# Optimization experiments

Hardware: AMD Instinct MI355X
Metric: run time of the kernel (lower is better)

## Reference

```python
import jax, jax.numpy as jnp
import numpy as np

BS, S, DIM, H = 4, 2048, 1024, 16
DH = DIM // H  # 64


def setup_inputs() -> dict:
    key = jax.random.key(0)
    ks = jax.random.split(key, 12)
    def lin(k, fan_in):
        bound = 1.0 / np.sqrt(fan_in)
        kw, kb = jax.random.split(k)
        W = jax.random.uniform(kw, (DIM, DIM), jnp.float32, -bound, bound)
        b = jax.random.uniform(kb, (DIM,), jnp.float32, -bound, bound)
        return W, b
    Wq, bq = lin(ks[0], DIM)
    Wk, bk = lin(ks[1], DIM)
    Wv, bv = lin(ks[2], DIM)
    Wo, bo = lin(ks[3], DIM)
    return {
        "query": jax.random.normal(ks[4], (BS, S, DIM), jnp.float32),
        "key": jax.random.normal(ks[5], (BS, S, DIM), jnp.float32),
        "value": jax.random.normal(ks[6], (BS, S, DIM), jnp.float32),
        "mask": jnp.ones((BS, S), jnp.int32),
        "Wq": Wq, "bq": bq, "Wk": Wk, "bk": bk,
        "Wv": Wv, "bv": bv, "Wo": Wo, "bo": bo,
    }


def reference(query, key, value, mask, Wq, bq, Wk, bk, Wv, bv, Wo, bo):
    bs, q_len, dim = query.shape
    def shape_heads(x):  # (bs, s, dim) -> (bs, H, s, DH)
        return x.reshape(bs, -1, H, DH).transpose(0, 2, 1, 3)
    # Linear projections (torch Linear: x @ W.T + b)
    q = shape_heads(query @ Wq.T + bq)
    k = shape_heads(key @ Wk.T + bk)
    v = shape_heads(value @ Wv.T + bv)
    q = q / jnp.sqrt(jnp.asarray(DH, q.dtype))
    # scores: (bs, H, q_len, k_len)
    scores = jnp.einsum('bhqd,bhkd->bhqk', q, k)
    neg = jnp.asarray(-jnp.inf, scores.dtype)
    pad = (mask == 0)[:, None, None, :]  # (bs,1,1,k_len)
    scores = jnp.where(pad, neg, scores)
    weights = jax.nn.softmax(scores, axis=-1)
    # dropout is identity in eval mode (reference is deterministic)
    context = jnp.einsum('bhqk,bhkd->bhqd', weights, v)
    context = context.transpose(0, 2, 1, 3).reshape(bs, q_len, dim)
    return context @ Wo.T + bo
```

## Files before the change

kernel.cpp:

```cpp
#include <hip/hip_runtime.h>
#include <hip/hip_bf16.h>
#include <math.h>

#define BSZ 4
#define SEQ 2048
#define DIMN 1024
#define NHEAD 16
#define DHEAD 64
#define MROWS (BSZ*SEQ)

typedef __bf16 bf16x8 __attribute__((ext_vector_type(8)));
typedef float  f32x4  __attribute__((ext_vector_type(4)));
typedef float  f32x16 __attribute__((ext_vector_type(16)));
typedef float  fvec4  __attribute__((ext_vector_type(4)));
typedef short  s16x4  __attribute__((ext_vector_type(4)));
typedef short  s16x8  __attribute__((ext_vector_type(8)));

__device__ __forceinline__ short f2bf(float v) {
  __hip_bfloat16 b = __float2bfloat16(v);
  return *reinterpret_cast<short*>(&b);
}
__device__ __forceinline__ float bf2f(short s) {
  __hip_bfloat16 b = *reinterpret_cast<__hip_bfloat16*>(&s);
  return __bfloat162float(b);
}

__device__ __forceinline__ void gld_lds16(const void* g, void* l) {
  __builtin_amdgcn_global_load_lds((const __attribute__((address_space(1))) void*)g,
                                   (__attribute__((address_space(3))) void*)l, 16, 0, 0);
}

#define QSC 0.18033688011112042f

__global__ __launch_bounds__(256) void pack_w4(
    const float* __restrict__ Wq, const float* __restrict__ Wk,
    const float* __restrict__ Wv, const float* __restrict__ Wo,
    short* __restrict__ WQh, short* __restrict__ WKh,
    short* __restrict__ WVh, short* __restrict__ WOh, short* __restrict__ WOl,
    long n)
{
  long i = ((long)blockIdx.x * 256 + threadIdx.x) * 4;
  if (i >= n) return;
  int which = blockIdx.y;
  if (which == 3) {
    fvec4 v = *(const fvec4*)&Wo[i];
    s16x4 h, l;
#pragma unroll
    for (int j = 0; j < 4; ++j) {
      short hb = f2bf(v[j]);
      h[j] = hb;
      l[j] = f2bf(v[j] - bf2f(hb));
    }
    *(s16x4*)&WOh[i] = h;
    *(s16x4*)&WOl[i] = l;
  } else {
    const float* src = which == 0 ? Wq : (which == 1 ? Wk : Wv);
    short* dst = which == 0 ? WQh : (which == 1 ? WKh : WVh);
    float sc = which == 0 ? QSC : 1.f;
    fvec4 v = *(const fvec4*)&src[i];
    s16x4 h;
#pragma unroll
    for (int j = 0; j < 4; ++j) h[j] = f2bf(v[j] * sc);
    *(s16x4*)&dst[i] = h;
  }
}

__global__ __launch_bounds__(256) void pack_hi3(
    const float* __restrict__ q, const float* __restrict__ k,
    const float* __restrict__ v,
    short* __restrict__ xq, short* __restrict__ xk, short* __restrict__ xv,
    long n)
{
  long i = ((long)blockIdx.x * 256 + threadIdx.x) * 4;
  if (i >= n) return;
  const float* src = blockIdx.y == 0 ? q : (blockIdx.y == 1 ? k : v);
  short* dst = blockIdx.y == 0 ? xq : (blockIdx.y == 1 ? xk : xv);
  fvec4 x = *(const fvec4*)&src[i];
  s16x4 h;
#pragma unroll
  for (int j = 0; j < 4; ++j) h[j] = f2bf(x[j]);
  *(s16x4*)&dst[i] = h;
}

__global__ __launch_bounds__(256) void maskbias_k(
    const int* __restrict__ mask, float* __restrict__ mb, int n)
{
  int i = blockIdx.x * 256 + threadIdx.x;
  if (i < n) mb[i] = mask[i] ? 0.f : -1e30f;
}

__global__ __launch_bounds__(64) void mask_flags(
    const int* __restrict__ mask, int* __restrict__ flg)
{
  int c = blockIdx.x;
  int base = (c >> 4) * SEQ + (c & 15) * 128;
  int m0 = mask[base + threadIdx.x];
  int m1 = mask[base + 64 + threadIdx.x];
  unsigned long long bal = __ballot(m0 != 0 && m1 != 0);
  if (threadIdx.x == 0) flg[c] = (bal == ~0ull) ? 1 : 0;
}

__global__ __launch_bounds__(256) void gemm_qkv(
    const short* __restrict__ XBq, const short* __restrict__ XBk,
    const short* __restrict__ XBv,
    const short* __restrict__ WQh, const short* __restrict__ WKh,
    const short* __restrict__ WVh,
    const float* __restrict__ bq, const float* __restrict__ bk,
    const float* __restrict__ bv,
    short* __restrict__ QB, short* __restrict__ KB, short* __restrict__ VTo)
{
  __shared__ __align__(16) short sA[128*32];
  __shared__ __align__(16) short sB[128*32];
  const int z = blockIdx.z;
  const short* A  = z == 0 ? XBq : (z == 1 ? XBk : XBv);
  const short* Bw = z == 0 ? WQh : (z == 1 ? WKh : WVh);
  const float* bias = z == 0 ? bq : (z == 1 ? bk : bv);
  short* Cb = z == 0 ? QB : (z == 1 ? KB : VTo);
  const float bscale = z == 0 ? QSC : 1.f;

  const int flat = blockIdx.y * 8 + blockIdx.x;
  const int nb = (flat & 7) * 64 + (flat >> 3);
  const int m0 = (nb >> 3) * 128, n0 = (nb & 7) * 128;

  const int t = threadIdx.x;
  const int ln = t & 15, quad = (t & 63) >> 4, w = t >> 6;
  const int wm = w >> 1, wn = w & 1;
  const int lrow = t >> 2;
  const int lko = (((t & 3) ^ ((t >> 3) & 3))) * 8;
  const int fsw = ((ln >> 1) & 3);
  f32x4 acc[4][4];
#pragma unroll
  for (int i = 0; i < 4; ++i)
#pragma unroll
    for (int j = 0; j < 4; ++j) acc[i][j] = (f32x4){0.f,0.f,0.f,0.f};

  for (int k0 = 0; k0 < DIMN; k0 += 32) {
    __syncthreads();
#pragma unroll
    for (int u = 0; u < 2; ++u) {
      int row = u*64 + lrow;
      gld_lds16(A  + (size_t)(m0+row)*DIMN + k0 + lko, sA + u*2048 + t*8);
      gld_lds16(Bw + (size_t)(n0+row)*DIMN + k0 + lko, sB + u*2048 + t*8);
    }
    __syncthreads();
    bf16x8 af[4], bfr[4];
#pragma unroll
    for (int mt = 0; mt < 4; ++mt)
      af[mt] = *(bf16x8*)&sA[(wm*64 + mt*16 + ln)*32 + (quad ^ fsw)*8];
#pragma unroll
    for (int nt = 0; nt < 4; ++nt)
      bfr[nt] = *(bf16x8*)&sB[(wn*64 + nt*16 + ln)*32 + (quad ^ fsw)*8];
#pragma unroll
    for (int mt = 0; mt < 4; ++mt)
#pragma unroll
      for (int nt = 0; nt < 4; ++nt)
        acc[mt][nt] = __builtin_amdgcn_mfma_f32_16x16x32_bf16(af[mt], bfr[nt], acc[mt][nt], 0, 0, 0);
  }
#pragma unroll
  for (int nt = 0; nt < 4; ++nt) {
    int col = n0 + wn*64 + nt*16 + ln;
    float bv2 = bias[col] * bscale;
    if (z == 2) {
      int hd = col >> 6, dd = col & 63;
#pragma unroll
      for (int mt = 0; mt < 4; ++mt) {
        int sg = m0 + wm*64 + mt*16 + quad*4;
        int b = sg >> 11, s = sg & 2047;
        s16x4 h;
#pragma unroll
        for (int r = 0; r < 4; ++r) h[r] = f2bf(acc[mt][nt][r] + bv2);
        *(s16x4*)&Cb[((size_t)((b*16 + hd)*64 + dd))*SEQ + s] = h;
      }
    } else {
#pragma unroll
      for (int mt = 0; mt < 4; ++mt)
#pragma unroll
        for (int r = 0; r < 4; ++r) {
          int row = m0 + wm*64 + mt*16 + quad*4 + r;
          Cb[(size_t)row*DIMN + col] = f2bf(acc[mt][nt][r] + bv2);
        }
    }
  }
}

__global__ __launch_bounds__(256) void gemm_sp(
    const short* __restrict__ Ah, const short* __restrict__ Al,
    const short* __restrict__ Bh, const short* __restrict__ Bl,
    const float* __restrict__ bias, float bscale,
    float* __restrict__ C, int M, int N, int K)
{
  __shared__ __align__(16) short sA[2*128*32];
  __shared__ __align__(16) short sB[2*128*32];
  const int t = threadIdx.x;
  const int ln = t & 15, quad = (t & 63) >> 4, w = t >> 6;
  const int wm = w >> 1, wn = w & 1;
  const int flat = blockIdx.y * 8 + blockIdx.x;
  const int nb = (flat & 7) * 64 + (flat >> 3);
  const int m0 = (nb >> 3) * 128, n0 = (nb & 7) * 128;
  const int lrow = t >> 2;
  const int lko = (((t & 3) ^ ((t >> 3) & 3))) * 8;
  const int fsw = ((ln >> 1) & 3);
  f32x4 acc[4][4];
#pragma unroll
  for (int i = 0; i < 4; ++i)
#pragma unroll
    for (int j = 0; j < 4; ++j) acc[i][j] = (f32x4){0.f,0.f,0.f,0.f};

  for (int k0 = 0; k0 < K; k0 += 32) {
    __syncthreads();
#pragma unroll
    for (int u = 0; u < 2; ++u) {
      int row = u*64 + lrow;
      gld_lds16(Ah + (size_t)(m0+row)*K + k0 + lko, sA + u*2048 + t*8);
      gld_lds16(Al + (size_t)(m0+row)*K + k0 + lko, sA + 4096 + u*2048 + t*8);
      gld_lds16(Bh + (size_t)(n0+row)*K + k0 + lko, sB + u*2048 + t*8);
      gld_lds16(Bl + (size_t)(n0+row)*K + k0 + lko, sB + 4096 + u*2048 + t*8);
    }
    __syncthreads();
    bf16x8 ah[4], al[4], bh[4], bl[4];
#pragma unroll
    for (int mt = 0; mt < 4; ++mt) {
      int r = wm*64 + mt*16 + ln;
      ah[mt] = *(bf16x8*)&sA[r*32 + (quad ^ fsw)*8];
      al[mt] = *(bf16x8*)&sA[4096 + r*32 + (quad ^ fsw)*8];
    }
#pragma unroll
    for (int nt = 0; nt < 4; ++nt) {
      int r = wn*64 + nt*16 + ln;
      bh[nt] = *(bf16x8*)&sB[r*32 + (quad ^ fsw)*8];
      bl[nt] = *(bf16x8*)&sB[4096 + r*32 + (quad ^ fsw)*8];
    }
#pragma unroll
    for (int mt = 0; mt < 4; ++mt)
#pragma unroll
      for (int nt = 0; nt < 4; ++nt) {
        acc[mt][nt] = __builtin_amdgcn_mfma_f32_16x16x32_bf16(ah[mt], bh[nt], acc[mt][nt], 0, 0, 0);
        acc[mt][nt] = __builtin_amdgcn_mfma_f32_16x16x32_bf16(ah[mt], bl[nt], acc[mt][nt], 0, 0, 0);
        acc[mt][nt] = __builtin_amdgcn_mfma_f32_16x16x32_bf16(al[mt], bh[nt], acc[mt][nt], 0, 0, 0);
      }
  }
#pragma unroll
  for (int nt = 0; nt < 4; ++nt) {
    float bv = bias[n0 + wn*64 + nt*16 + ln] * bscale;
#pragma unroll
    for (int mt = 0; mt < 4; ++mt)
#pragma unroll
      for (int r = 0; r < 4; ++r)
        C[(size_t)(m0 + wm*64 + mt*16 + quad*4 + r)*N + (n0 + wn*64 + nt*16 + ln)] =
            acc[mt][nt][r] + bv;
  }
}

__global__ __launch_bounds__(256, 3) void attn_32(
    const short* __restrict__ QB, const short* __restrict__ KB,
    const short* __restrict__ VT, const float* __restrict__ mb,
    const int* __restrict__ flg,
    short* __restrict__ CTXh, short* __restrict__ CTXl)
{
  __shared__ __align__(16) short lds[16384];
  short* sK = lds;
  short* sV = lds + 8192;

  const int t = threadIdx.x;
  const int l31 = t & 31, hi = (t >> 5) & 1, w = t >> 6;
  const int gb = blockIdx.x;
  const int chunk = gb >> 3, qt128 = chunk & 15, bh = ((chunk >> 4) << 3) + (gb & 7);
  const int b = bh >> 4, hd = bh & 15;

#pragma unroll
  for (int i = 0; i < 4; ++i) {
    int u = i*256 + t;
    int row = u >> 3, gr = (u & 7) ^ (row & 7);
    gld_lds16(QB + ((size_t)(b*SEQ + qt128*128 + row))*DIMN + hd*64 + gr*8,
              sK + u*8);
  }
  __syncthreads();
  const int q = w*32 + l31;
  bf16x8 qf[4];
#pragma unroll
  for (int ks = 0; ks < 4; ++ks)
    qf[ks] = *(bf16x8*)&sK[q*64 + ((ks*2 + hi) ^ (q & 7))*8];

  f32x16 o_acc[2] = {};
  float m_run = -1e30f, l_run = 0.f;

  for (int kt = 0; kt < SEQ/128; ++kt) {
    __syncthreads();
#pragma unroll
    for (int i = 0; i < 4; ++i) {
      int u = i*256 + t;
      { int row = u >> 3, gr = (u & 7) ^ (row & 7);
        gld_lds16(KB + ((size_t)(b*SEQ + kt*128 + row))*DIMN + hd*64 + gr*8,
                  sK + u*8); }
      { int d = u >> 4, gr = (u & 15) ^ (d & 15);
        gld_lds16(VT + ((size_t)(bh*64 + d))*SEQ + kt*128 + gr*8,
                  sV + u*8); }
    }
    __syncthreads();

    f32x16 sacc[4] = {};
#pragma unroll
    for (int ks = 0; ks < 4; ++ks)
#pragma unroll
      for (int mt = 0; mt < 4; ++mt) {
        int kc = mt*32 + l31;
        bf16x8 kf = *(bf16x8*)&sK[kc*64 + ((ks*2 + hi) ^ (kc & 7))*8];
        sacc[mt] = __builtin_amdgcn_mfma_f32_32x32x16_bf16(kf, qf[ks], sacc[mt], 0, 0, 0);
      }

    if (!flg[b*16 + kt]) {
#pragma unroll
      for (int mt = 0; mt < 4; ++mt)
#pragma unroll
        for (int r = 0; r < 16; ++r)
          sacc[mt][r] += mb[b*SEQ + kt*128 + mt*32 + (r&3) + 8*(r>>2) + 4*hi];
    }

    float tmax = -1e30f;
#pragma unroll
    for (int mt = 0; mt < 4; ++mt)
#pragma unroll
      for (int r = 0; r < 16; ++r) tmax = fmaxf(tmax, sacc[mt][r]);
    tmax = fmaxf(tmax, __shfl_xor(tmax, 32));

    if (!__all(tmax <= m_run + 8.f)) {
      float mnew = fmaxf(m_run, tmax);
      float alpha = exp2f(m_run - mnew);
      l_run *= alpha;
#pragma unroll
      for (int dt = 0; dt < 2; ++dt)
#pragma unroll
        for (int r = 0; r < 16; ++r) o_acc[dt][r] *= alpha;
      m_run = mnew;
    }

    float rs = 0.f;
#pragma unroll
    for (int mt = 0; mt < 4; ++mt)
#pragma unroll
      for (int r = 0; r < 16; ++r) {
        float p = exp2f(sacc[mt][r] - m_run);
        sacc[mt][r] = p;
        rs += p;
      }
    rs += __shfl_xor(rs, 32);
    l_run += rs;

#pragma unroll
    for (int mt = 0; mt < 4; ++mt) {
      unsigned wv[8];
#pragma unroll
      for (int i = 0; i < 8; ++i) {
        float plo = sacc[mt][2*i], phi = sacc[mt][2*i+1];
        asm("v_cvt_pk_bf16_f32 %0, %1, %2" : "=v"(wv[i]) : "v"(plo), "v"(phi));
      }
#pragma unroll
      for (int h = 0; h < 2; ++h) {
        unsigned f0 = wv[h*4+0], f1 = wv[h*4+1], f2 = wv[h*4+2], f3 = wv[h*4+3];
        asm volatile("v_permlane32_swap_b32 %0, %1" : "+v"(f0), "+v"(f2));
        asm volatile("v_permlane32_swap_b32 %0, %1" : "+v"(f1), "+v"(f3));
        union { unsigned u[4]; bf16x8 v; } pu;
        pu.u[0] = f0; pu.u[1] = f1; pu.u[2] = f2; pu.u[3] = f3;
        const int kcs = mt*2 + h;
#pragma unroll
        for (int dt = 0; dt < 2; ++dt) {
          int d = dt*32 + l31;
          bf16x8 vf = *(bf16x8*)&sV[d*128 + ((kcs*2 + hi) ^ (d & 15))*8];
          o_acc[dt] = __builtin_amdgcn_mfma_f32_32x32x16_bf16(vf, pu.v, o_acc[dt], 0, 0, 0);
        }
      }
    }
  }

  float invl = (l_run > 0.f) ? 1.f / l_run : 0.f;
  const size_t rowbase = (size_t)(b*SEQ + qt128*128 + q)*DIMN + hd*64;
#pragma unroll
  for (int dt = 0; dt < 2; ++dt)
#pragma unroll
    for (int rg = 0; rg < 4; ++rg) {
      s16x4 hq, lq;
#pragma unroll
      for (int r2 = 0; r2 < 4; ++r2) {
        float val = o_acc[dt][rg*4 + r2] * invl;
        short hb = f2bf(val);
        hq[r2] = hb;
        lq[r2] = f2bf(val - bf2f(hb));
      }
      size_t idx = rowbase + dt*32 + rg*8 + hi*4;
      *(s16x4*)&CTXh[idx] = hq;
      *(s16x4*)&CTXl[idx] = lq;
    }
}

__global__ __launch_bounds__(256) void gemm_bt(
    const float* __restrict__ X, const float* __restrict__ W,
    const float* __restrict__ bias, float* __restrict__ C,
    int M, int N, int K)
{
  __shared__ __align__(16) float Xs[16][68];
  __shared__ __align__(16) float Ws[16][68];
  const int t  = threadIdx.x;
  const int tx = t & 15, ty = t >> 4;
  const int m0 = blockIdx.y << 6, n0 = blockIdx.x << 6;
  const int ldr = t >> 2;
  const int lk  = (t & 3) << 2;
  float acc[4][4] = {{0.f}};
  const float* Xp = X + (size_t)(m0 + ldr) * K + lk;
  const float* Wp = W + (size_t)(n0 + ldr) * K + lk;
  for (int k0 = 0; k0 < K; k0 += 16) {
    float4 xa = *(const float4*)(Xp + k0);
    float4 wa = *(const float4*)(Wp + k0);
    Xs[lk+0][ldr]=xa.x; Xs[lk+1][ldr]=xa.y; Xs[lk+2][ldr]=xa.z; Xs[lk+3][ldr]=xa.w;
    Ws[lk+0][ldr]=wa.x; Ws[lk+1][ldr]=wa.y; Ws[lk+2][ldr]=wa.z; Ws[lk+3][ldr]=wa.w;
    __syncthreads();
#pragma unroll
    for (int kk = 0; kk < 16; ++kk) {
      float4 a4 = *(const float4*)&Xs[kk][ty<<2];
      float4 b4 = *(const float4*)&Ws[kk][tx<<2];
      float av[4] = {a4.x, a4.y, a4.z, a4.w};
      float bv[4] = {b4.x, b4.y, b4.z, b4.w};
#pragma unroll
      for (int i = 0; i < 4; ++i)
#pragma unroll
        for (int j = 0; j < 4; ++j)
          acc[i][j] = fmaf(av[i], bv[j], acc[i][j]);
    }
    __syncthreads();
  }
  float4 bb4 = *(const float4*)&bias[n0 + (tx<<2)];
  const float bv[4] = {bb4.x, bb4.y, bb4.z, bb4.w};
#pragma unroll
  for (int i = 0; i < 4; ++i) {
    float4 o;
    o.x = acc[i][0]+bv[0]; o.y = acc[i][1]+bv[1];
    o.z = acc[i][2]+bv[2]; o.w = acc[i][3]+bv[3];
    *(float4*)&C[(size_t)(m0 + (ty<<2) + i) * N + n0 + (tx<<2)] = o;
  }
}

__global__ __launch_bounds__(256) void attn_fwd(
    const float* __restrict__ Q, const float* __restrict__ Kbuf,
    const float* __restrict__ Vbuf, const int* __restrict__ mask,
    float* __restrict__ CTX)
{
  __shared__ __align__(16) float Qs[64][68];
  __shared__ __align__(16) float KPs[64][68];
  __shared__ __align__(16) float Vs[64][68];
  const int t  = threadIdx.x;
  const int tx = t & 15, ty = t >> 4;
  const int qt = blockIdx.x;
  const int bh = blockIdx.y;
  const int b  = bh >> 4, h = bh & 15;
  const int ldr = t >> 2;
  const int lcb = (t & 3) << 2;
  const float* Qp = Q + (size_t)(b*SEQ + (qt<<6)) * DIMN + h*DHEAD;
#pragma unroll
  for (int u = 0; u < 4; ++u) {
    int kb = lcb + (u<<4);
    float4 q4 = *(const float4*)(Qp + (size_t)ldr*DIMN + kb);
    Qs[kb+0][ldr]=q4.x; Qs[kb+1][ldr]=q4.y; Qs[kb+2][ldr]=q4.z; Qs[kb+3][ldr]=q4.w;
  }
  float mrow[4], lsum[4], o[4][4];
#pragma unroll
  for (int i = 0; i < 4; ++i) {
    mrow[i] = -1e30f; lsum[i] = 0.f;
#pragma unroll
    for (int j = 0; j < 4; ++j) o[i][j] = 0.f;
  }
  const int qrow0 = ty << 2;
  const int col0  = tx << 2;
  for (int kt = 0; kt < SEQ/64; ++kt) {
    __syncthreads();
    const float* Kp = Kbuf + (size_t)(b*SEQ + (kt<<6)) * DIMN + h*DHEAD;
    const float* Vp = Vbuf + (size_t)(b*SEQ + (kt<<6)) * DIMN + h*DHEAD;
#pragma unroll
    for (int u = 0; u < 4; ++u) {
      int kb = lcb + (u<<4);
      float4 k4 = *(const float4*)(Kp + (size_t)ldr*DIMN + kb);
      KPs[kb+0][ldr]=k4.x; KPs[kb+1][ldr]=k4.y; KPs[kb+2][ldr]=k4.z; KPs[kb+3][ldr]=k4.w;
      float4 v4 = *(const float4*)(Vp + (size_t)ldr*DIMN + kb);
      *(float4*)&Vs[ldr][kb] = v4;
    }
    __syncthreads();
    float s[4][4] = {{0.f}};
#pragma unroll 8
    for (int kk = 0; kk < 64; ++kk) {
      float4 a4 = *(const float4*)&Qs[kk][qrow0];
      float4 b4 = *(const float4*)&KPs[kk][col0];
      float av[4] = {a4.x, a4.y, a4.z, a4.w};
      float bv[4] = {b4.x, b4.y, b4.z, b4.w};
#pragma unroll
      for (int i = 0; i < 4; ++i)
#pragma unroll
        for (int j = 0; j < 4; ++j)
          s[i][j] = fmaf(av[i], bv[j], s[i][j]);
    }
    int mk[4];
#pragma unroll
    for (int j = 0; j < 4; ++j) mk[j] = mask[b*SEQ + (kt<<6) + col0 + j];
    float p[4][4];
#pragma unroll
    for (int i = 0; i < 4; ++i) {
#pragma unroll
      for (int j = 0; j < 4; ++j)
        s[i][j] = mk[j] ? s[i][j]*0.125f : -1e30f;
      float tm = fmaxf(fmaxf(s[i][0], s[i][1]), fmaxf(s[i][2], s[i][3]));
#pragma unroll
      for (int off = 8; off >= 1; off >>= 1)
        tm = fmaxf(tm, __shfl_xor(tm, off, 64));
      float mnew  = fmaxf(mrow[i], tm);
      float aa = __expf(mrow[i] - mnew);
      mrow[i] = mnew;
      float rsum = 0.f;
#pragma unroll
      for (int j = 0; j < 4; ++j) {
        float pv = __expf(s[i][j] - mnew);
        p[i][j] = pv; rsum += pv;
      }
#pragma unroll
      for (int off = 8; off >= 1; off >>= 1)
        rsum += __shfl_xor(rsum, off, 64);
      lsum[i] = lsum[i]*aa + rsum;
#pragma unroll
      for (int j = 0; j < 4; ++j) o[i][j] *= aa;
    }
    __syncthreads();
#pragma unroll
    for (int i = 0; i < 4; ++i)
#pragma unroll
      for (int j = 0; j < 4; ++j)
        KPs[col0 + j][qrow0 + i] = p[i][j];
    __syncthreads();
#pragma unroll 8
    for (int kk = 0; kk < 64; ++kk) {
      float4 a4 = *(const float4*)&KPs[kk][qrow0];
      float4 v4 = *(const float4*)&Vs[kk][col0];
      float av[4] = {a4.x, a4.y, a4.z, a4.w};
      float vv[4] = {v4.x, v4.y, v4.z, v4.w};
#pragma unroll
      for (int i = 0; i < 4; ++i)
#pragma unroll
        for (int j = 0; j < 4; ++j)
          o[i][j] = fmaf(av[i], vv[j], o[i][j]);
    }
  }
  float* Cp = CTX + (size_t)(b*SEQ + (qt<<6)) * DIMN + h*DHEAD;
#pragma unroll
  for (int i = 0; i < 4; ++i) {
    float inv = lsum[i] > 0.f ? 1.0f/lsum[i] : 0.f;
    float4 ov;
    ov.x = o[i][0]*inv; ov.y = o[i][1]*inv;
    ov.z = o[i][2]*inv; ov.w = o[i][3]*inv;
    *(float4*)(Cp + (size_t)(qrow0 + i)*DIMN + col0) = ov;
  }
}

extern "C" void kernel_launch(void* const* d_in, const int* in_sizes, int n_in,
                              void* d_out, int out_size, void* d_ws, size_t ws_size,
                              hipStream_t stream)
{
  const float* query = (const float*)d_in[0];
  const float* key   = (const float*)d_in[1];
  const float* value = (const float*)d_in[2];
  const int*   mask  = (const int*)d_in[3];
  const float* Wq = (const float*)d_in[4];
  const float* bq = (const float*)d_in[5];
  const float* Wk = (const float*)d_in[6];
  const float* bk = (const float*)d_in[7];
  const float* Wv = (const float*)d_in[8];
  const float* bv = (const float*)d_in[9];
  const float* Wo = (const float*)d_in[10];
  const float* bo = (const float*)d_in[11];
  float* out = (float*)d_out;

  const size_t E  = (size_t)MROWS * DIMN;
  const size_t WE = (size_t)DIMN * DIMN;

  const size_t o_XB   = 5*WE*2;
  const size_t o_QB   = o_XB   + 3*E*2;
  const size_t o_KB   = o_QB   + E*2;
  const size_t o_VT   = o_KB   + E*2;
  const size_t o_CTXh = o_VT   + E*2;
  const size_t o_CTXl = o_CTXh + E*2;
  const size_t o_MB   = o_CTXl + E*2;
  const size_t o_FLG  = o_MB   + MROWS*4;
  const size_t NEED   = o_FLG  + 64*4;

  if (ws_size < NEED) {
    const size_t n = E;
    float* Qb = (float*)d_ws;
    float* Kb = Qb + n;
    float* Vb = Kb + n;
    float* Cb = Vb + n;
    dim3 gg(DIMN/64, MROWS/64), blk(256);
    hipLaunchKernelGGL(gemm_bt, gg, blk, 0, stream, query, Wq, bq, Qb, MROWS, DIMN, DIMN);
    hipLaunchKernelGGL(gemm_bt, gg, blk, 0, stream, key,   Wk, bk, Kb, MROWS, DIMN, DIMN);
    hipLaunchKernelGGL(gemm_bt, gg, blk, 0, stream, value, Wv, bv, Vb, MROWS, DIMN, DIMN);
    dim3 ga(SEQ/64, BSZ*NHEAD);
    hipLaunchKernelGGL(attn_fwd, ga, blk, 0, stream, Qb, Kb, Vb, mask, Cb);
    hipLaunchKernelGGL(gemm_bt, gg, blk, 0, stream, Cb, Wo, bo, out, MROWS, DIMN, DIMN);
    return;
  }

  char* Wp = (char*)d_ws;
  short* WQh = (short*)Wp;
  short* WKh = WQh + WE;
  short* WVh = WQh + 2*WE;
  short* WOh = WQh + 3*WE;
  short* WOl = WQh + 4*WE;
  short* XBq  = (short*)(Wp + o_XB);
  short* XBk  = XBq + E;
  short* XBv  = XBk + E;
  short* QB   = (short*)(Wp + o_QB);
  short* KB   = (short*)(Wp + o_KB);
  short* VT   = (short*)(Wp + o_VT);
  short* CTXh = (short*)(Wp + o_CTXh);
  short* CTXl = (short*)(Wp + o_CTXl);
  float* MB   = (float*)(Wp + o_MB);
  int*   FLG  = (int*)(Wp + o_FLG);

  dim3 blk(256);
  dim3 gW(WE/1024, 4), gX(E/1024, 3);
  dim3 gqkv(DIMN/128, MROWS/128, 3);
  dim3 gg(DIMN/128, MROWS/128);
  dim3 gat(BSZ*NHEAD*SEQ/128);

  hipLaunchKernelGGL(pack_w4, gW, blk, 0, stream, Wq, Wk, Wv, Wo,
                     WQh, WKh, WVh, WOh, WOl, (long)WE);
  hipLaunchKernelGGL(maskbias_k, dim3(MROWS/256), blk, 0, stream, mask, MB, MROWS);
  hipLaunchKernelGGL(mask_flags, dim3(64), dim3(64), 0, stream, mask, FLG);
  hipLaunchKernelGGL(pack_hi3, gX, blk, 0, stream, query, key, value,
                     XBq, XBk, XBv, (long)E);

  hipLaunchKernelGGL(gemm_qkv, gqkv, blk, 0, stream,
                     XBq, XBk, XBv, WQh, WKh, WVh, bq, bk, bv, QB, KB, VT);

  hipLaunchKernelGGL(attn_32, gat, blk, 0, stream, QB, KB, VT, MB, FLG, CTXh, CTXl);

  hipLaunchKernelGGL(gemm_sp, gg, blk, 0, stream, CTXh, CTXl, WOh, WOl, bo, 1.f,
                     out, MROWS, DIMN, DIMN);
}
```

Before: 417.6 us.

## Switch projection GEMMs to 32x32x16 MFMA with 64-wide K tiles

Both the QKV projection GEMM and the split-precision output GEMM move from 16x16x32 MFMA tiles to 32x32x16 MFMA tiles. The K step per iteration grows from 32 to 64, with a new XOR-swizzled LDS layout, so there are half as many barrier pairs and more math per LDS fragment load. The cost is doubled shared memory per block, which may lower occupancy. The epilogue indexing is rewritten to match the 32x32 accumulator layout.

```diff
diff --git a/kernel.cpp b/kernel.cpp
--- a/kernel.cpp
+++ b/kernel.cpp
@@ -109,8 +109,8 @@
     const float* __restrict__ bv,
     short* __restrict__ QB, short* __restrict__ KB, short* __restrict__ VTo)
 {
-  __shared__ __align__(16) short sA[128*32];
-  __shared__ __align__(16) short sB[128*32];
+  __shared__ __align__(16) short sA[128*64];
+  __shared__ __align__(16) short sB[128*64];
   const int z = blockIdx.z;
   const short* A  = z == 0 ? XBq : (z == 1 ? XBk : XBv);
   const short* Bw = z == 0 ? WQh : (z == 1 ? WKh : WVh);
@@ -123,62 +123,66 @@
   const int m0 = (nb >> 3) * 128, n0 = (nb & 7) * 128;
 
   const int t = threadIdx.x;
-  const int ln = t & 15, quad = (t & 63) >> 4, w = t >> 6;
+  const int l31 = t & 31, hi = (t >> 5) & 1, w = t >> 6;
   const int wm = w >> 1, wn = w & 1;
-  const int lrow = t >> 2;
-  const int lko = (((t & 3) ^ ((t >> 3) & 3))) * 8;
-  const int fsw = ((ln >> 1) & 3);
-  f32x4 acc[4][4];
-#pragma unroll
-  for (int i = 0; i < 4; ++i)
-#pragma unroll
-    for (int j = 0; j < 4; ++j) acc[i][j] = (f32x4){0.f,0.f,0.f,0.f};
-
-  for (int k0 = 0; k0 < DIMN; k0 += 32) {
-    __syncthreads();
-#pragma unroll
-    for (int u = 0; u < 2; ++u) {
-      int row = u*64 + lrow;
-      gld_lds16(A  + (size_t)(m0+row)*DIMN + k0 + lko, sA + u*2048 + t*8);
-      gld_lds16(Bw + (size_t)(n0+row)*DIMN + k0 + lko, sB + u*2048 + t*8);
-    }
-    __syncthreads();
-    bf16x8 af[4], bfr[4];
-#pragma unroll
-    for (int mt = 0; mt < 4; ++mt)
-      af[mt] = *(bf16x8*)&sA[(wm*64 + mt*16 + ln)*32 + (quad ^ fsw)*8];
-#pragma unroll
-    for (int nt = 0; nt < 4; ++nt)
-      bfr[nt] = *(bf16x8*)&sB[(wn*64 + nt*16 + ln)*32 + (quad ^ fsw)*8];
-#pragma unroll
-    for (int mt = 0; mt < 4; ++mt)
-#pragma unroll
-      for (int nt = 0; nt < 4; ++nt)
-        acc[mt][nt] = __builtin_amdgcn_mfma_f32_16x16x32_bf16(af[mt], bfr[nt], acc[mt][nt], 0, 0, 0);
-  }
-#pragma unroll
-  for (int nt = 0; nt < 4; ++nt) {
-    int col = n0 + wn*64 + nt*16 + ln;
+  const int srow7 = (t >> 3) & 7;
+  const int sg = (t & 7) ^ srow7;
+  int offF[4];
+#pragma unroll
+  for (int ks = 0; ks < 4; ++ks)
+    offF[ks] = l31*64 + ((ks*2 + hi) ^ (l31 & 7))*8;
+
+  f32x16 acc[2][2] = {};
+
+  for (int k0 = 0; k0 < DIMN; k0 += 64) {
+    __syncthreads();
+#pragma unroll
+    for (int i = 0; i < 4; ++i) {
+      int row = i*32 + (t >> 3);
+      gld_lds16(A  + (size_t)(m0+row)*DIMN + k0 + sg*8, sA + (i*256 + t)*8);
+      gld_lds16(Bw + (size_t)(n0+row)*DIMN + k0 + sg*8, sB + (i*256 + t)*8);
+    }
+    __syncthreads();
+#pragma unroll
+    for (int ks = 0; ks < 4; ++ks) {
+      bf16x8 af0 = *(const bf16x8*)&sA[wm*4096 + offF[ks]];
+      bf16x8 af1 = *(const bf16x8*)&sA[wm*4096 + 2048 + offF[ks]];
+      bf16x8 bf0 = *(const bf16x8*)&sB[wn*4096 + offF[ks]];
+      bf16x8 bf1 = *(const bf16x8*)&sB[wn*4096 + 2048 + offF[ks]];
+      acc[0][0] = __builtin_amdgcn_mfma_f32_32x32x16_bf16(af0, bf0, acc[0][0], 0, 0, 0);
+      acc[0][1] = __builtin_amdgcn_mfma_f32_32x32x16_bf16(af0, bf1, acc[0][1], 0, 0, 0);
+      acc[1][0] = __builtin_amdgcn_mfma_f32_32x32x16_bf16(af1, bf0, acc[1][0], 0, 0, 0);
+      acc[1][1] = __builtin_amdgcn_mfma_f32_32x32x16_bf16(af1, bf1, acc[1][1], 0, 0, 0);
+    }
+  }
+
+#pragma unroll
+  for (int nt = 0; nt < 2; ++nt) {
+    int col = n0 + wn*64 + nt*32 + l31;
     float bv2 = bias[col] * bscale;
     if (z == 2) {
       int hd = col >> 6, dd = col & 63;
 #pragma unroll
-      for (int mt = 0; mt < 4; ++mt) {
-        int sg = m0 + wm*64 + mt*16 + quad*4;
-        int b = sg >> 11, s = sg & 2047;
-        s16x4 h;
-#pragma unroll
-        for (int r = 0; r < 4; ++r) h[r] = f2bf(acc[mt][nt][r] + bv2);
-        *(s16x4*)&Cb[((size_t)((b*16 + hd)*64 + dd))*SEQ + s] = h;
-      }
+      for (int mt = 0; mt < 2; ++mt)
+#pragma unroll
+        for (int rg = 0; rg < 4; ++rg) {
+          int sgr = m0 + wm*64 + mt*32 + rg*8 + hi*4;
+          int b = sgr >> 11, s = sgr & 2047;
+          s16x4 h;
+#pragma unroll
+          for (int r2 = 0; r2 < 4; ++r2) h[r2] = f2bf(acc[mt][nt][rg*4+r2] + bv2);
+          *(s16x4*)&Cb[((size_t)((b*16 + hd)*64 + dd))*SEQ + s] = h;
+        }
     } else {
 #pragma unroll
-      for (int mt = 0; mt < 4; ++mt)
-#pragma unroll
-        for (int r = 0; r < 4; ++r) {
-          int row = m0 + wm*64 + mt*16 + quad*4 + r;
-          Cb[(size_t)row*DIMN + col] = f2bf(acc[mt][nt][r] + bv2);
-        }
+      for (int mt = 0; mt < 2; ++mt)
+#pragma unroll
+        for (int rg = 0; rg < 4; ++rg)
+#pragma unroll
+          for (int r2 = 0; r2 < 4; ++r2) {
+            int row = m0 + wm*64 + mt*32 + rg*8 + hi*4 + r2;
+            Cb[(size_t)row*DIMN + col] = f2bf(acc[mt][nt][rg*4+r2] + bv2);
+          }
     }
   }
 }
@@ -189,65 +193,72 @@
     const float* __restrict__ bias, float bscale,
     float* __restrict__ C, int M, int N, int K)
 {
-  __shared__ __align__(16) short sA[2*128*32];
-  __shared__ __align__(16) short sB[2*128*32];
+  __shared__ __align__(16) short sA[2*128*64];
+  __shared__ __align__(16) short sB[2*128*64];
   const int t = threadIdx.x;
-  const int ln = t & 15, quad = (t & 63) >> 4, w = t >> 6;
+  const int l31 = t & 31, hi = (t >> 5) & 1, w = t >> 6;
   const int wm = w >> 1, wn = w & 1;
   const int flat = blockIdx.y * 8 + blockIdx.x;
   const int nb = (flat & 7) * 64 + (flat >> 3);
   const int m0 = (nb >> 3) * 128, n0 = (nb & 7) * 128;
-  const int lrow = t >> 2;
-  const int lko = (((t & 3) ^ ((t >> 3) & 3))) * 8;
-  const int fsw = ((ln >> 1) & 3);
-  f32x4 acc[4][4];
-#pragma unroll
-  for (int i = 0; i < 4; ++i)
-#pragma unroll
-    for (int j = 0; j < 4; ++j) acc[i][j] = (f32x4){0.f,0.f,0.f,0.f};
-
-  for (int k0 = 0; k0 < K; k0 += 32) {
-    __syncthreads();
-#pragma unroll
-    for (int u = 0; u < 2; ++u) {
-      int row = u*64 + lrow;
-      gld_lds16(Ah + (size_t)(m0+row)*K + k0 + lko, sA + u*2048 + t*8);
-      gld_lds16(Al + (size_t)(m0+row)*K + k0 + lko, sA + 4096 + u*2048 + t*8);
-      gld_lds16(Bh + (size_t)(n0+row)*K + k0 + lko, sB + u*2048 + t*8);
-      gld_lds16(Bl + (size_t)(n0+row)*K + k0 + lko, sB + 4096 + u*2048 + t*8);
-    }
-    __syncthreads();
-    bf16x8 ah[4], al[4], bh[4], bl[4];
-#pragma unroll
-    for (int mt = 0; mt < 4; ++mt) {
-      int r = wm*64 + mt*16 + ln;
-      ah[mt] = *(bf16x8*)&sA[r*32 + (quad ^ fsw)*8];
-      al[mt] = *(bf16x8*)&sA[4096 + r*32 + (quad ^ fsw)*8];
-    }
-#pragma unroll
-    for (int nt = 0; nt < 4; ++nt) {
-      int r = wn*64 + nt*16 + ln;
-      bh[nt] = *(bf16x8*)&sB[r*32 + (quad ^ fsw)*8];
-      bl[nt] = *(bf16x8*)&sB[4096 + r*32 + (quad ^ fsw)*8];
-    }
-#pragma unroll
-    for (int mt = 0; mt < 4; ++mt)
-#pragma unroll
-      for (int nt = 0; nt < 4; ++nt) {
-        acc[mt][nt] = __builtin_amdgcn_mfma_f32_16x16x32_bf16(ah[mt], bh[nt], acc[mt][nt], 0, 0, 0);
-        acc[mt][nt] = __builtin_amdgcn_mfma_f32_16x16x32_bf16(ah[mt], bl[nt], acc[mt][nt], 0, 0, 0);
-        acc[mt][nt] = __builtin_amdgcn_mfma_f32_16x16x32_bf16(al[mt], bh[nt], acc[mt][nt], 0, 0, 0);
-      }
-  }
-#pragma unroll
-  for (int nt = 0; nt < 4; ++nt) {
-    float bv = bias[n0 + wn*64 + nt*16 + ln] * bscale;
-#pragma unroll
-    for (int mt = 0; mt < 4; ++mt)
-#pragma unroll
-      for (int r = 0; r < 4; ++r)
-        C[(size_t)(m0 + wm*64 + mt*16 + quad*4 + r)*N + (n0 + wn*64 + nt*16 + ln)] =
-            acc[mt][nt][r] + bv;
+  const int sg = (t & 7) ^ ((t >> 3) & 7);
+  int offF[4];
+#pragma unroll
+  for (int ks = 0; ks < 4; ++ks)
+    offF[ks] = l31*64 + ((ks*2 + hi) ^ (l31 & 7))*8;
+
+  f32x16 acc[2][2] = {};
+
+  for (int k0 = 0; k0 < K; k0 += 64) {
+    __syncthreads();
+#pragma unroll
+    for (int i = 0; i < 4; ++i) {
+      int row = i*32 + (t >> 3);
+      int u8 = (i*256 + t)*8;
+      gld_lds16(Ah + (size_t)(m0+row)*K + k0 + sg*8, sA + u8);
+      gld_lds16(Al + (size_t)(m0+row)*K + k0 + sg*8, sA + 8192 + u8);
+      gld_lds16(Bh + (size_t)(n0+row)*K + k0 + sg*8, sB + u8);
+      gld_lds16(Bl + (size_t)(n0+row)*K + k0 + sg*8, sB + 8192 + u8);
+    }
+    __syncthreads();
+#pragma unroll
+    for (int ks = 0; ks < 4; ++ks) {
+      bf16x8 ah0 = *(const bf16x8*)&sA[wm*4096 + offF[ks]];
+      bf16x8 ah1 = *(const bf16x8*)&sA[wm*4096 + 2048 + offF[ks]];
+      bf16x8 al0 = *(const bf16x8*)&sA[8192 + wm*4096 + offF[ks]];
+      bf16x8 al1 = *(const bf16x8*)&sA[8192 + wm*4096 + 2048 + offF[ks]];
+      bf16x8 bh0 = *(const bf16x8*)&sB[wn*4096 + offF[ks]];
+      bf16x8 bh1 = *(const bf16x8*)&sB[wn*4096 + 2048 + offF[ks]];
+      bf16x8 bl0 = *(const bf16x8*)&sB[8192 + wn*4096 + offF[ks]];
+      bf16x8 bl1 = *(const bf16x8*)&sB[8192 + wn*4096 + 2048 + offF[ks]];
+      acc[0][0] = __builtin_amdgcn_mfma_f32_32x32x16_bf16(ah0, bh0, acc[0][0], 0, 0, 0);
+      acc[0][0] = __builtin_amdgcn_mfma_f32_32x32x16_bf16(ah0, bl0, acc[0][0], 0, 0, 0);
+      acc[0][0] = __builtin_amdgcn_mfma_f32_32x32x16_bf16(al0, bh0, acc[0][0], 0, 0, 0);
+      acc[0][1] = __builtin_amdgcn_mfma_f32_32x32x16_bf16(ah0, bh1, acc[0][1], 0, 0, 0);
+      acc[0][1] = __builtin_amdgcn_mfma_f32_32x32x16_bf16(ah0, bl1, acc[0][1], 0, 0, 0);
+      acc[0][1] = __builtin_amdgcn_mfma_f32_32x32x16_bf16(al0, bh1, acc[0][1], 0, 0, 0);
+      acc[1][0] = __builtin_amdgcn_mfma_f32_32x32x16_bf16(ah1, bh0, acc[1][0], 0, 0, 0);
+      acc[1][0] = __builtin_amdgcn_mfma_f32_32x32x16_bf16(ah1, bl0, acc[1][0], 0, 0, 0);
+      acc[1][0] = __builtin_amdgcn_mfma_f32_32x32x16_bf16(al1, bh0, acc[1][0], 0, 0, 0);
+      acc[1][1] = __builtin_amdgcn_mfma_f32_32x32x16_bf16(ah1, bh1, acc[1][1], 0, 0, 0);
+      acc[1][1] = __builtin_amdgcn_mfma_f32_32x32x16_bf16(ah1, bl1, acc[1][1], 0, 0, 0);
+      acc[1][1] = __builtin_amdgcn_mfma_f32_32x32x16_bf16(al1, bh1, acc[1][1], 0, 0, 0);
+    }
+  }
+
+#pragma unroll
+  for (int nt = 0; nt < 2; ++nt) {
+    int col = n0 + wn*64 + nt*32 + l31;
+    float bv = bias[col] * bscale;
+#pragma unroll
+    for (int mt = 0; mt < 2; ++mt)
+#pragma unroll
+      for (int rg = 0; rg < 4; ++rg)
+#pragma unroll
+        for (int r2 = 0; r2 < 4; ++r2) {
+          int row = m0 + wm*64 + mt*32 + rg*8 + hi*4 + r2;
+          C[(size_t)row*N + col] = acc[mt][nt][rg*4+r2] + bv;
+        }
   }
 }
 
```

Result: faster. 399.6 us (-4.3%).
